# Kernel optimization log

Measured on AMD Instinct MI355X. Metric: run time of the kernel, lower is better.

Reference implementation:

```python
import jax, jax.numpy as jnp
import numpy as np

N = 50000      # n_points (== n_support, non-strided)
H = 32         # neighbors per point
IN_F = 128
OUT_F = 256
MID = OUT_F // 4   # bottleneck width = 64
K = 15         # kernel points
RADIUS = 2.0
KP_EXTENT = 1.2 * RADIUS / 5.0  # config.KP_extent * radius / density_parameter
EPS = 1e-6
SLOPE = 0.1


def _wvar(k, size):
    # weight_variable: normal(scale=sqrt(2/size[-1])), zeroed outside 2*std
    std = np.sqrt(2.0 / size[-1])
    w = jax.random.normal(k, size, jnp.float32) * std
    return jnp.where(jnp.abs(w) > 2.0 * std, 0.0, w)


def setup_inputs():
    key = jax.random.key(0)
    ks = jax.random.split(key, 12)
    query_points = jax.random.uniform(ks[0], (N, 3), jnp.float32)
    support_points = query_points  # non-strided: same cloud
    neighbors_indices = jax.random.randint(ks[1], (N, H), 0, N, jnp.int32)
    features = jax.random.normal(ks[2], (N, IN_F), jnp.float32)
    kp = (jax.random.uniform(ks[3], (K, 3), jnp.float32) * 2.0 - 1.0) * (0.66 * KP_EXTENT)
    kernel_points = kp.at[0].set(0.0)  # fixed_kernel_points='center'
    w1 = _wvar(ks[4], (IN_F, MID))
    kw = _wvar(ks[5], (K, MID, MID))
    w3 = _wvar(ks[6], (MID, OUT_F))
    ws = _wvar(ks[7], (IN_F, OUT_F))
    def bnp(k, c):
        k1, k2 = jax.random.split(k)
        g = jax.random.uniform(k1, (c,), jnp.float32, 0.75, 1.25)
        b = jax.random.normal(k2, (c,), jnp.float32) * 0.1
        return g, b
    g1, b1 = bnp(ks[8], MID)
    g2, b2 = bnp(ks[9], MID)
    g3, b3 = bnp(ks[10], OUT_F)
    gs, bs = bnp(ks[11], OUT_F)
    return dict(query_points=query_points, support_points=support_points,
                neighbors_indices=neighbors_indices, features=features,
                kernel_points=kernel_points, w1=w1, g1=g1, b1=b1,
                kw=kw, g2=g2, b2=b2, w3=w3, g3=g3, b3=b3, ws=ws, gs=gs, bs=bs)


def _bn(x, g, b):
    # BatchNorm1d in training mode: batch statistics over points, biased var
    m = jnp.mean(x, 0)
    v = jnp.var(x, 0)
    return g * (x - m) * jax.lax.rsqrt(v + EPS) + b


def _lrelu(x):
    return jnp.where(x >= 0, x, SLOPE * x)


def _unary(x, w, g, b):
    return _lrelu(_bn(x @ w, g, b))


def _kpconv(q, s, inds, f, kp, kw):
    # pad support with a far shadow point and features with a zero row (faithful to KPConv)
    s_pad = jnp.concatenate([s, jnp.full((1, 3), 1e6, s.dtype)], 0)
    f_pad = jnp.concatenate([f, jnp.zeros((1, f.shape[1]), f.dtype)], 0)
    neigh = s_pad[inds]                        # [n,h,3] gather
    d = neigh - q[:, None, :]                  # [n,h,3]
    sq = jnp.sum((d[:, :, None, :] - kp[None, None, :, :]) ** 2, -1)  # [n,h,K]
    dist = jnp.sqrt(jnp.maximum(sq, 1e-12))
    infl = jnp.maximum(0.0, 1.0 - dist / KP_EXTENT)   # 'linear' KP_influence
    nf = f_pad[inds]                           # [n,h,d] gather
    wf = jnp.einsum('nhk,nhd->nkd', infl, nf)  # aggregate over neighbors
    return jnp.einsum('nkd,kdo->no', wf, kw)   # 'sum' aggregation over kernel pts


def reference(query_points, support_points, neighbors_indices, features, kernel_points,
              w1, g1, b1, kw, g2, b2, w3, g3, b3, ws, gs, bs):
    x = _unary(features, w1, g1, b1)                                     # conv1
    x = _lrelu(_bn(_kpconv(query_points, support_points, neighbors_indices,
                           x, kernel_points, kw), g2, b2))               # conv2 (KPConv)
    x = _unary(x, w3, g3, b3)                                            # conv3
    sc = _unary(features, ws, gs, bs)                                    # shortcut (non-strided)
    return _lrelu(sc + x)
```

## Files before the change

kernel.cpp:

```cpp
#include <hip/hip_runtime.h>

#define NPTS 50000
#define HN 32
#define INF1 128
#define OUTF3 256
#define MIDF 64
#define KP 15
#define EPSV 1e-6f
#define SLOPE 0.1f
#define KPE 0.48f
#define INVN (1.f / 50000.f)

typedef __attribute__((ext_vector_type(8))) short short8;
typedef __attribute__((ext_vector_type(4))) float float4v;
typedef unsigned short ushort;
typedef unsigned long long ull;

__device__ inline ushort f2bf(float f) {
    union { float f; unsigned u; } v; v.f = f;
    unsigned r = v.u + 0x7fff + ((v.u >> 16) & 1);
    return (ushort)(r >> 16);
}
__device__ inline float bf2f(ushort u) {
    union { unsigned u; float f; } v; v.u = ((unsigned)u) << 16;
    return v.f;
}
__device__ inline unsigned cvt_pk_bf16(float lo, float hi) {
    unsigned r;
    asm("v_cvt_pk_bf16_f32 %0, %1, %2" : "=v"(r) : "v"(lo), "v"(hi));
    return r;
}


__global__ __launch_bounds__(256)
void k_repack_all(const float* __restrict__ w1, const float* __restrict__ wsw,
                  ushort* __restrict__ wpC,
                  const float* __restrict__ kw, ushort* __restrict__ wpk,
                  const float* __restrict__ w3, ushort* __restrict__ wp3) {
    int id = blockIdx.x * 256 + threadIdx.x;
    if (id < 5120) {
        int l = id & 63;
        int nt = (id >> 6) % 20, s = id / 1280;
        int n = nt * 16 + (l & 15);
        int k0 = s * 32 + ((l >> 4) & 3) * 8;
#pragma unroll
        for (int j = 0; j < 8; j++) {
            float v = (n < 64) ? w1[(k0 + j) * 64 + n] : wsw[(k0 + j) * 256 + (n - 64)];
            wpC[id * 8 + j] = f2bf(v);
        }
    } else if (id < 13312) {
        int id2 = id - 5120;
        int l2 = id2 & 63;
        int nt = (id2 >> 6) & 3, s = id2 >> 8;
        int n = nt * 16 + (l2 & 15);
        int kd0 = s * 32 + ((l2 >> 4) & 3) * 8;
#pragma unroll
        for (int j = 0; j < 8; j++) {
            int kd = kd0 + j, d = kd >> 4, kk = kd & 15;
            float v = (kk < KP) ? kw[kk * 4096 + d * 64 + n] : 0.f;
            wpk[id2 * 8 + j] = f2bf(v);
        }
    } else if (id < 15360) {
        int id3 = id - 13312;
        int l3 = id3 & 63;
        int nt = (id3 >> 6) % 16, s = id3 / 1024;
        int n = nt * 16 + (l3 & 15);
        int k0 = s * 32 + ((l3 >> 4) & 3) * 8;
#pragma unroll
        for (int j = 0; j < 8; j++)
            wp3[id3 * 8 + j] = f2bf(w3[(k0 + j) * 256 + n]);
    }
}

__global__ __launch_bounds__(256)
void k_conv1sc(const float* __restrict__ feat, const ushort* __restrict__ WpC,
               ushort* __restrict__ x1raw, ushort* __restrict__ scb,
               float* __restrict__ Sa1, float* __restrict__ Sq1,
               float* __restrict__ SaS, float* __restrict__ SqS, int M) {
    __shared__ float sred[320], qred[320];
    int t = threadIdx.x;
    int w = t >> 6, l = t & 63;
    int dl = l & 15, q4 = l >> 4;

    for (int c = t; c < 320; c += 256) { sred[c] = 0.f; qred[c] = 0.f; }
    __syncthreads();

    int m0 = blockIdx.x * 64 + w * 16;
    int row = m0 + dl;
    long arow = (row < M) ? row : (M - 1);
    const float* ap0 = feat + arow * INF1 + q4 * 8;
    short8 afr[4];
#pragma unroll
    for (int s = 0; s < 4; s++) {
        float4 a0 = *(const float4*)(ap0 + s * 32);
        float4 a1 = *(const float4*)(ap0 + s * 32 + 4);
        union { short8 v; unsigned d[4]; } au;
        au.d[0] = cvt_pk_bf16(a0.x, a0.y);
        au.d[1] = cvt_pk_bf16(a0.z, a0.w);
        au.d[2] = cvt_pk_bf16(a1.x, a1.y);
        au.d[3] = cvt_pk_bf16(a1.z, a1.w);
        afr[s] = au.v;
    }
    const short8* Bp = (const short8*)WpC + l;
    int rb = q4 * 4;
#pragma unroll
    for (int half = 0; half < 2; half++) {
        float4v acc[10];
#pragma unroll
        for (int j = 0; j < 10; j++) acc[j] = (float4v){0.f, 0.f, 0.f, 0.f};
#pragma unroll
        for (int s = 0; s < 4; s++)
#pragma unroll
            for (int j = 0; j < 10; j++) {
                short8 bf = Bp[(s * 20 + half * 10 + j) * 64];
                acc[j] = __builtin_amdgcn_mfma_f32_16x16x32_bf16(afr[s], bf, acc[j], 0, 0, 0);
            }
#pragma unroll
        for (int r = 0; r < 4; r++) {
            int rr = m0 + rb + r;
            if (rr < M) {
                if (half == 0) {
                    uint2 pk;
                    pk.x = cvt_pk_bf16(acc[0][r], acc[1][r]);
                    pk.y = cvt_pk_bf16(acc[2][r], acc[3][r]);
                    *(uint2*)(x1raw + (long)rr * 64 + 4 * dl) = pk;
#pragma unroll
                    for (int j = 4; j < 10; j++)
                        scb[(long)rr * 256 + (j * 16 + dl - 64)] = f2bf(acc[j][r]);
                } else {
#pragma unroll
                    for (int j = 0; j < 10; j++)
                        scb[(long)rr * 256 + ((10 + j) * 16 + dl - 64)] = f2bf(acc[j][r]);
                }
            }
        }
#pragma unroll
        for (int j = 0; j < 10; j++) {
            float s = 0.f, q = 0.f;
#pragma unroll
            for (int r = 0; r < 4; r++) {
                float v = ((m0 + rb + r) < M) ? acc[j][r] : 0.f;
                s += v; q += v * v;
            }
            s += __shfl_xor(s, 16); s += __shfl_xor(s, 32);
            q += __shfl_xor(q, 16); q += __shfl_xor(q, 32);
            if (q4 == 0) {
                atomicAdd(&sred[(half * 10 + j) * 16 + dl], s);
                atomicAdd(&qred[(half * 10 + j) * 16 + dl], q);
            }
        }
    }
    __syncthreads();
    for (int c = t; c < 320; c += 256) {
        if (c < 64) { atomicAdd(&Sa1[c], sred[c]); atomicAdd(&Sq1[c], qred[c]); }
        else        { atomicAdd(&SaS[c - 64], sred[c]); atomicAdd(&SqS[c - 64], qred[c]); }
    }
}

__global__ __launch_bounds__(256)
void k_bnx(const ushort* __restrict__ X, ushort* __restrict__ Y,
           const float* __restrict__ Sa, const float* __restrict__ Sq,
           const float* __restrict__ g, const float* __restrict__ b) {
    __shared__ float sc[64], sh[64];
    int t = threadIdx.x;
    if (t < 64) {
        float m = Sa[t] * INVN;
        float v = Sq[t] * INVN - m * m;
        float s = g[t] * rsqrtf(v + EPSV);
        sc[t] = s; sh[t] = b[t] - s * m;
    }
    __syncthreads();
    int i = blockIdx.x * 256 + t;
    long base = (long)i * 4;
    int dlp = i & 15;
    ull vin = *(const ull*)(X + base);
    float vv[4];
#pragma unroll
    for (int j = 0; j < 4; j++) {
        int c = j * 16 + dlp;
        float f = bf2f((ushort)((vin >> (16 * j)) & 0xffff));
        float v = f * sc[c] + sh[c];
        vv[j] = (v >= 0.f) ? v : SLOPE * v;
    }
    uint2 vo;
    vo.x = cvt_pk_bf16(vv[0], vv[1]);
    vo.y = cvt_pk_bf16(vv[2], vv[3]);
    *(uint2*)(Y + base) = vo;
}

__global__ __launch_bounds__(256)
void k_kpconv(const float* __restrict__ qpts, const float* __restrict__ spts,
              const int* __restrict__ nbr, const ushort* __restrict__ x1b,
              const float* __restrict__ kpp, const ushort* __restrict__ kwp,
              ushort* __restrict__ y, float* __restrict__ Sa, float* __restrict__ Sq) {
    __shared__ __align__(16) ushort wfs[16][1032];
    __shared__ float posd[4][4][3][HN];

    int t = threadIdx.x;
    int w = t >> 6, l = t & 63;
    int dl = l & 15, q4 = l >> 4;

    int kmin = (dl < KP) ? dl : (KP - 1);
    float kx = kpp[kmin * 3 + 0], ky = kpp[kmin * 3 + 1], kz = kpp[kmin * 3 + 2];

    int nb = blockIdx.x * 16 + w * 4;

    int idg[4][8];
#pragma unroll
    for (int pp = 0; pp < 4; pp++) {
        const int4* np = (const int4*)(nbr + (long)(nb + pp) * HN + q4 * 8);
        int4 ia = np[0], ib = np[1];
        idg[pp][0] = ia.x; idg[pp][1] = ia.y; idg[pp][2] = ia.z; idg[pp][3] = ia.w;
        idg[pp][4] = ib.x; idg[pp][5] = ib.y; idg[pp][6] = ib.z; idg[pp][7] = ib.w;
    }

    {
        int hh = l & 31, hf = l >> 5;
        float dx[2], dy[2], dz[2];
#pragma unroll
        for (int p2 = 0; p2 < 2; p2++) {
            int pp = hf * 2 + p2;
            int idx = nbr[(long)(nb + pp) * HN + hh];
            dx[p2] = spts[(long)idx * 3 + 0] - qpts[(nb + pp) * 3 + 0];
            dy[p2] = spts[(long)idx * 3 + 1] - qpts[(nb + pp) * 3 + 1];
            dz[p2] = spts[(long)idx * 3 + 2] - qpts[(nb + pp) * 3 + 2];
        }
#pragma unroll
        for (int p2 = 0; p2 < 2; p2++) {
            int pp = hf * 2 + p2;
            posd[w][pp][0][hh] = dx[p2];
            posd[w][pp][1][hh] = dy[p2];
            posd[w][pp][2][hh] = dz[p2];
        }
    }

    uint2 rj[4][8];
#pragma unroll
    for (int pp = 0; pp < 4; pp++)
#pragma unroll
        for (int j = 0; j < 8; j++)
            rj[pp][j] = *(const uint2*)(x1b + (long)idg[pp][j] * MIDF + 4 * dl);

#pragma unroll
    for (int pp = 0; pp < 4; pp++) {
        union { float4 v; float f[4]; } px0, px1, py0, py1, pz0, pz1;
        px0.v = *(const float4*)&posd[w][pp][0][q4 * 8];
        px1.v = *(const float4*)&posd[w][pp][0][q4 * 8 + 4];
        py0.v = *(const float4*)&posd[w][pp][1][q4 * 8];
        py1.v = *(const float4*)&posd[w][pp][1][q4 * 8 + 4];
        pz0.v = *(const float4*)&posd[w][pp][2][q4 * 8];
        pz1.v = *(const float4*)&posd[w][pp][2][q4 * 8 + 4];

        float inf[8];
#pragma unroll
        for (int j = 0; j < 8; j++) {
            float ex = ((j < 4) ? px0.f[j & 3] : px1.f[j & 3]) - kx;
            float ey = ((j < 4) ? py0.f[j & 3] : py1.f[j & 3]) - ky;
            float ez = ((j < 4) ? pz0.f[j & 3] : pz1.f[j & 3]) - kz;
            float sq = ex * ex + ey * ey + ez * ez;
            float dist = sqrtf(fmaxf(sq, 1e-12f));
            inf[j] = fmaxf(0.f, 1.f - dist * (1.f / KPE));
        }
        union { short8 v; unsigned d2[4]; } afr;
#pragma unroll
        for (int jj = 0; jj < 4; jj++)
            afr.d2[jj] = cvt_pk_bf16(inf[2 * jj], inf[2 * jj + 1]);

        union { short8 v; unsigned d[4]; } bfr[4];
#pragma unroll
        for (int dj = 0; dj < 4; dj++) {
            unsigned a_lo = rj[pp][2 * dj].x, b_lo = rj[pp][2 * dj + 1].x;
            unsigned a_hi = rj[pp][2 * dj].y, b_hi = rj[pp][2 * dj + 1].y;
            bfr[0].d[dj] = __builtin_amdgcn_perm(b_lo, a_lo, 0x05040100u);
            bfr[1].d[dj] = __builtin_amdgcn_perm(b_lo, a_lo, 0x07060302u);
            bfr[2].d[dj] = __builtin_amdgcn_perm(b_hi, a_hi, 0x05040100u);
            bfr[3].d[dj] = __builtin_amdgcn_perm(b_hi, a_hi, 0x07060302u);
        }

        float4v wfa[4];
#pragma unroll
        for (int nt = 0; nt < 4; nt++)
            wfa[nt] = __builtin_amdgcn_mfma_f32_16x16x32_bf16(
                afr.v, bfr[nt].v, (float4v){0.f, 0.f, 0.f, 0.f}, 0, 0, 0);

        int p = w * 4 + pp;
#pragma unroll
        for (int nt = 0; nt < 4; nt++) {
            uint2 pk;
            pk.x = cvt_pk_bf16(wfa[nt][0], wfa[nt][1]);
            pk.y = cvt_pk_bf16(wfa[nt][2], wfa[nt][3]);
            *(uint2*)(&wfs[p][(nt * 16 + dl) * 16 + q4 * 4]) = pk;
        }
    }

    const short8* Bq = (const short8*)kwp + l;
    short8 bc0 = Bq[(0 * 4 + w) * 64];
    short8 bc1 = Bq[(1 * 4 + w) * 64];
    __syncthreads();

    float4v acc0 = (float4v){0.f, 0.f, 0.f, 0.f};
    float4v acc1 = (float4v){0.f, 0.f, 0.f, 0.f};
    const ushort* arow = &wfs[dl][0] + q4 * 8;
#pragma unroll
    for (int s = 0; s < 32; s += 2) {
        short8 bn0, bn1;
        if (s < 30) {
            bn0 = Bq[((s + 2) * 4 + w) * 64];
            bn1 = Bq[((s + 3) * 4 + w) * 64];
        }
        short8 a0 = *(const short8*)(arow + s * 32);
        short8 a1 = *(const short8*)(arow + (s + 1) * 32);
        acc0 = __builtin_amdgcn_mfma_f32_16x16x32_bf16(a0, bc0, acc0, 0, 0, 0);
        acc1 = __builtin_amdgcn_mfma_f32_16x16x32_bf16(a1, bc1, acc1, 0, 0, 0);
        bc0 = bn0; bc1 = bn1;
    }
    float4v acc = acc0 + acc1;

    int o = w * 16 + dl;
    float s = 0.f, q = 0.f;
#pragma unroll
    for (int r = 0; r < 4; r++) {
        float v = acc[r];
        y[(long)(blockIdx.x * 16 + q4 * 4 + r) * MIDF + o] = f2bf(v);
        s += v; q += v * v;
    }
    s += __shfl_xor(s, 16); s += __shfl_xor(s, 32);
    q += __shfl_xor(q, 16); q += __shfl_xor(q, 32);
    if (q4 == 0) {
        atomicAdd(&Sa[o], s);
        atomicAdd(&Sq[o], q);
    }
}

__global__ __launch_bounds__(256)
void k_conv3(const ushort* __restrict__ x2raw, const ushort* __restrict__ Wp,
             ushort* __restrict__ x3b,
             const float* __restrict__ Sa2, const float* __restrict__ Sq2,
             const float* __restrict__ g2, const float* __restrict__ b2,
             float* __restrict__ Sa3, float* __restrict__ Sq3, int M) {
    __shared__ float sred[256], qred[256];
    __shared__ float scs[64], shs[64];
    int t = threadIdx.x;
    int w = t >> 6, l = t & 63;
    int dl = l & 15, q4 = l >> 4;

    if (t < 64) {
        float m = Sa2[t] * INVN;
        float v = Sq2[t] * INVN - m * m;
        float s = g2[t] * rsqrtf(v + EPSV);
        scs[t] = s; shs[t] = b2[t] - s * m;
    }
    sred[t] = 0.f; qred[t] = 0.f;
    __syncthreads();

    int m0 = blockIdx.x * 64 + w * 16;
    int row = m0 + dl;
    long arow = (row < M) ? row : (M - 1);
    const ushort* ap0 = x2raw + arow * MIDF + q4 * 8;
    short8 au2[2];
#pragma unroll
    for (int s = 0; s < 2; s++) {
        union { short8 v; ushort u[8]; } raw;
        union { short8 v; unsigned d[4]; } cv;
        raw.v = *(const short8*)(ap0 + s * 32);
        float fv[8];
#pragma unroll
        for (int e = 0; e < 8; e++) {
            int d = s * 32 + q4 * 8 + e;
            float f = bf2f(raw.u[e]) * scs[d] + shs[d];
            fv[e] = (f >= 0.f) ? f : SLOPE * f;
        }
#pragma unroll
        for (int e2 = 0; e2 < 4; e2++)
            cv.d[e2] = cvt_pk_bf16(fv[2 * e2], fv[2 * e2 + 1]);
        au2[s] = cv.v;
    }
    const short8* Bp = (const short8*)Wp + l;
    int rb = q4 * 4;
#pragma unroll
    for (int half = 0; half < 2; half++) {
        float4v acc[8];
#pragma unroll
        for (int j = 0; j < 8; j++) acc[j] = (float4v){0.f, 0.f, 0.f, 0.f};
#pragma unroll
        for (int s = 0; s < 2; s++)
#pragma unroll
            for (int j = 0; j < 8; j++) {
                short8 bf = Bp[(s * 16 + half * 8 + j) * 64];
                acc[j] = __builtin_amdgcn_mfma_f32_16x16x32_bf16(au2[s], bf, acc[j], 0, 0, 0);
            }
#pragma unroll
        for (int r = 0; r < 4; r++) {
            int rr = m0 + rb + r;
            if (rr < M) {
#pragma unroll
                for (int j = 0; j < 8; j++)
                    x3b[(long)rr * 256 + (half * 8 + j) * 16 + dl] = f2bf(acc[j][r]);
            }
        }
#pragma unroll
        for (int j = 0; j < 8; j++) {
            float s = 0.f, q = 0.f;
#pragma unroll
            for (int r = 0; r < 4; r++) {
                float v = ((m0 + rb + r) < M) ? acc[j][r] : 0.f;
                s += v; q += v * v;
            }
            s += __shfl_xor(s, 16); s += __shfl_xor(s, 32);
            q += __shfl_xor(q, 16); q += __shfl_xor(q, 32);
            if (q4 == 0) {
                atomicAdd(&sred[(half * 8 + j) * 16 + dl], s);
                atomicAdd(&qred[(half * 8 + j) * 16 + dl], q);
            }
        }
    }
    __syncthreads();
    atomicAdd(&Sa3[t], sred[t]);
    atomicAdd(&Sq3[t], qred[t]);
}

__global__ __launch_bounds__(256)
void k_final(const ushort* __restrict__ x3b, const ushort* __restrict__ scb,
             float* __restrict__ out,
             const float* __restrict__ a3, const float* __restrict__ q3,
             const float* __restrict__ g3, const float* __restrict__ b3,
             const float* __restrict__ aS, const float* __restrict__ qS,
             const float* __restrict__ gs, const float* __restrict__ bs) {
    __shared__ float s3[256], h3[256], sS[256], hS[256];
    int t = threadIdx.x;
    {
        float m = a3[t] * INVN;
        float v = q3[t] * INVN - m * m;
        float s = g3[t] * rsqrtf(v + EPSV);
        s3[t] = s; h3[t] = b3[t] - s * m;
        m = aS[t] * INVN;
        v = qS[t] * INVN - m * m;
        s = gs[t] * rsqrtf(v + EPSV);
        sS[t] = s; hS[t] = bs[t] - s * m;
    }
    __syncthreads();
    long i = (long)(blockIdx.x * 256 + t) * 4;
    int c0 = (int)(i & 255);
    ull va = *(const ull*)(x3b + i);
    ull vb = *(const ull*)(scb + i);
    float r[4];
#pragma unroll
    for (int j = 0; j < 4; j++) {
        int c = c0 + j;
        float x = bf2f((ushort)((va >> (16 * j)) & 0xffff)) * s3[c] + h3[c];
        x = (x >= 0.f) ? x : SLOPE * x;
        float sc = bf2f((ushort)((vb >> (16 * j)) & 0xffff)) * sS[c] + hS[c];
        sc = (sc >= 0.f) ? sc : SLOPE * sc;
        float v = x + sc;
        r[j] = (v >= 0.f) ? v : SLOPE * v;
    }
    *(float4*)(out + i) = (float4){r[0], r[1], r[2], r[3]};
}

extern "C" void kernel_launch(void* const* d_in, const int* in_sizes, int n_in,
                              void* d_out, int out_size, void* d_ws, size_t ws_size,
                              hipStream_t stream) {
    const float* qp   = (const float*)d_in[0];
    const float* sp   = (const float*)d_in[1];
    const int*   nbr  = (const int*)d_in[2];
    const float* feat = (const float*)d_in[3];
    const float* kpp  = (const float*)d_in[4];
    const float* w1   = (const float*)d_in[5];
    const float* g1   = (const float*)d_in[6];
    const float* b1   = (const float*)d_in[7];
    const float* kw   = (const float*)d_in[8];
    const float* g2   = (const float*)d_in[9];
    const float* b2   = (const float*)d_in[10];
    const float* w3   = (const float*)d_in[11];
    const float* g3   = (const float*)d_in[12];
    const float* b3   = (const float*)d_in[13];
    const float* wsw  = (const float*)d_in[14];
    const float* gs   = (const float*)d_in[15];
    const float* bs   = (const float*)d_in[16];
    float* out = (float*)d_out;

    char* base = (char*)d_ws;
    ushort* x1raw = (ushort*)(base + 0);
    ushort* x1b   = (ushort*)(base + 6400000);
    ushort* x2raw = (ushort*)(base + 12800000);
    ushort* x3b   = (ushort*)(base + 19200000);
    ushort* scb   = (ushort*)(base + 44800000);
    ushort* wpC   = (ushort*)(base + 70400000);
    ushort* wpk   = (ushort*)(base + 70481920);
    ushort* wp3   = (ushort*)(base + 70612992);
    float*  st    = (float*)(base + 70645760);
    float* acc1 = st,       *q1 = st + 64;
    float* acc2 = st + 128, *q2 = st + 192;
    float* acc3 = st + 256, *q3 = st + 512;
    float* accS = st + 768, *qS = st + 1024;

    hipMemsetAsync(st, 0, 1280 * sizeof(float), stream);

    k_repack_all<<<60, 256, 0, stream>>>(w1, wsw, wpC, kw, wpk, w3, wp3);

    k_conv1sc<<<782, 256, 0, stream>>>(feat, wpC, x1raw, scb, acc1, q1, accS, qS, NPTS);
    k_bnx<<<3125, 256, 0, stream>>>(x1raw, x1b, acc1, q1, g1, b1);

    k_kpconv<<<NPTS / 16, 256, 0, stream>>>(qp, sp, nbr, x1b, kpp, wpk, x2raw, acc2, q2);

    k_conv3<<<782, 256, 0, stream>>>(x2raw, wp3, x3b, acc2, q2, g2, b2, acc3, q3, NPTS);

    k_final<<<12500, 256, 0, stream>>>(x3b, scb, out, acc3, q3, g3, b3, accS, qS, gs, bs);
}
```

Baseline: 299.2 us.

## Recompute conv3 GEMM in final kernel instead of storing x3 intermediate

Splits conv3 into a stats-only pass that computes the GEMM and accumulates batch-norm sums without writing x3. A second pass recomputes the same small GEMM, stages the tile in shared memory, and applies BN, leaky ReLU and the residual add with the shortcut directly. This removes the 25.6MB bf16 write and re-read of x3 in exchange for doing the 64x256 GEMM twice. The 32KB shared tile may also reduce occupancy.

Measured after the change: 298.3 us. No clear change (-0.3%).

```diff
diff --git a/kernel.cpp b/kernel.cpp
--- a/kernel.cpp
+++ b/kernel.cpp
@@ -333,11 +333,10 @@
 }
 
 __global__ __launch_bounds__(256)
-void k_conv3(const ushort* __restrict__ x2raw, const ushort* __restrict__ Wp,
-             ushort* __restrict__ x3b,
-             const float* __restrict__ Sa2, const float* __restrict__ Sq2,
-             const float* __restrict__ g2, const float* __restrict__ b2,
-             float* __restrict__ Sa3, float* __restrict__ Sq3, int M) {
+void k_conv3stats(const ushort* __restrict__ x2raw, const ushort* __restrict__ Wp,
+                  const float* __restrict__ Sa2, const float* __restrict__ Sq2,
+                  const float* __restrict__ g2, const float* __restrict__ b2,
+                  float* __restrict__ Sa3, float* __restrict__ Sq3, int M) {
     __shared__ float sred[256], qred[256];
     __shared__ float scs[64], shs[64];
     int t = threadIdx.x;
@@ -390,15 +389,6 @@
                 acc[j] = __builtin_amdgcn_mfma_f32_16x16x32_bf16(au2[s], bf, acc[j], 0, 0, 0);
             }
 #pragma unroll
-        for (int r = 0; r < 4; r++) {
-            int rr = m0 + rb + r;
-            if (rr < M) {
-#pragma unroll
-                for (int j = 0; j < 8; j++)
-                    x3b[(long)rr * 256 + (half * 8 + j) * 16 + dl] = f2bf(acc[j][r]);
-            }
-        }
-#pragma unroll
         for (int j = 0; j < 8; j++) {
             float s = 0.f, q = 0.f;
 #pragma unroll
@@ -420,14 +410,28 @@
 }
 
 __global__ __launch_bounds__(256)
-void k_final(const ushort* __restrict__ x3b, const ushort* __restrict__ scb,
-             float* __restrict__ out,
-             const float* __restrict__ a3, const float* __restrict__ q3,
-             const float* __restrict__ g3, const float* __restrict__ b3,
-             const float* __restrict__ aS, const float* __restrict__ qS,
-             const float* __restrict__ gs, const float* __restrict__ bs) {
+void k_conv3final(const ushort* __restrict__ x2raw, const ushort* __restrict__ Wp,
+                  const ushort* __restrict__ scb, float* __restrict__ out,
+                  const float* __restrict__ Sa2, const float* __restrict__ Sq2,
+                  const float* __restrict__ g2, const float* __restrict__ b2,
+                  const float* __restrict__ a3, const float* __restrict__ q3,
+                  const float* __restrict__ g3, const float* __restrict__ b3,
+                  const float* __restrict__ aS, const float* __restrict__ qS,
+                  const float* __restrict__ gs, const float* __restrict__ bs,
+                  int M) {
+    __shared__ float scs[64], shs[64];
     __shared__ float s3[256], h3[256], sS[256], hS[256];
+    __shared__ __align__(8) ushort x3t[64][256];
     int t = threadIdx.x;
+    int w = t >> 6, l = t & 63;
+    int dl = l & 15, q4 = l >> 4;
+
+    if (t < 64) {
+        float m = Sa2[t] * INVN;
+        float v = Sq2[t] * INVN - m * m;
+        float s = g2[t] * rsqrtf(v + EPSV);
+        scs[t] = s; shs[t] = b2[t] - s * m;
+    }
     {
         float m = a3[t] * INVN;
         float v = q3[t] * INVN - m * m;
@@ -439,22 +443,76 @@
         sS[t] = s; hS[t] = bs[t] - s * m;
     }
     __syncthreads();
-    long i = (long)(blockIdx.x * 256 + t) * 4;
-    int c0 = (int)(i & 255);
-    ull va = *(const ull*)(x3b + i);
-    ull vb = *(const ull*)(scb + i);
-    float r[4];
-#pragma unroll
-    for (int j = 0; j < 4; j++) {
-        int c = c0 + j;
-        float x = bf2f((ushort)((va >> (16 * j)) & 0xffff)) * s3[c] + h3[c];
-        x = (x >= 0.f) ? x : SLOPE * x;
-        float sc = bf2f((ushort)((vb >> (16 * j)) & 0xffff)) * sS[c] + hS[c];
-        sc = (sc >= 0.f) ? sc : SLOPE * sc;
-        float v = x + sc;
-        r[j] = (v >= 0.f) ? v : SLOPE * v;
-    }
-    *(float4*)(out + i) = (float4){r[0], r[1], r[2], r[3]};
+
+    int m0 = blockIdx.x * 64 + w * 16;
+    int row = m0 + dl;
+    long arow = (row < M) ? row : (M - 1);
+    const ushort* ap0 = x2raw + arow * MIDF + q4 * 8;
+    short8 au2[2];
+#pragma unroll
+    for (int s = 0; s < 2; s++) {
+        union { short8 v; ushort u[8]; } raw;
+        union { short8 v; unsigned d[4]; } cv;
+        raw.v = *(const short8*)(ap0 + s * 32);
+        float fv[8];
+#pragma unroll
+        for (int e = 0; e < 8; e++) {
+            int d = s * 32 + q4 * 8 + e;
+            float f = bf2f(raw.u[e]) * scs[d] + shs[d];
+            fv[e] = (f >= 0.f) ? f : SLOPE * f;
+        }
+#pragma unroll
+        for (int e2 = 0; e2 < 4; e2++)
+            cv.d[e2] = cvt_pk_bf16(fv[2 * e2], fv[2 * e2 + 1]);
+        au2[s] = cv.v;
+    }
+    const short8* Bp = (const short8*)Wp + l;
+    int rb = q4 * 4;
+#pragma unroll
+    for (int half = 0; half < 2; half++) {
+        float4v acc[8];
+#pragma unroll
+        for (int j = 0; j < 8; j++) acc[j] = (float4v){0.f, 0.f, 0.f, 0.f};
+#pragma unroll
+        for (int s = 0; s < 2; s++)
+#pragma unroll
+            for (int j = 0; j < 8; j++) {
+                short8 bf = Bp[(s * 16 + half * 8 + j) * 64];
+                acc[j] = __builtin_amdgcn_mfma_f32_16x16x32_bf16(au2[s], bf, acc[j], 0, 0, 0);
+            }
+#pragma unroll
+        for (int r = 0; r < 4; r++) {
+            int lrow = w * 16 + rb + r;
+#pragma unroll
+            for (int j = 0; j < 8; j++)
+                x3t[lrow][(half * 8 + j) * 16 + dl] = f2bf(acc[j][r]);
+        }
+    }
+    __syncthreads();
+
+#pragma unroll
+    for (int it = 0; it < 16; it++) {
+        int e = it * 1024 + t * 4;
+        int lrow = e >> 8;
+        int grow = blockIdx.x * 64 + lrow;
+        if (grow < M) {
+            int col = e & 255;
+            ull va = *(const ull*)&x3t[lrow][col];
+            ull vb = *(const ull*)(scb + (long)grow * 256 + col);
+            float r[4];
+#pragma unroll
+            for (int j = 0; j < 4; j++) {
+                int c = col + j;
+                float x = bf2f((ushort)((va >> (16 * j)) & 0xffff)) * s3[c] + h3[c];
+                x = (x >= 0.f) ? x : SLOPE * x;
+                float sc = bf2f((ushort)((vb >> (16 * j)) & 0xffff)) * sS[c] + hS[c];
+                sc = (sc >= 0.f) ? sc : SLOPE * sc;
+                float v = x + sc;
+                r[j] = (v >= 0.f) ? v : SLOPE * v;
+            }
+            *(float4*)(out + (long)grow * 256 + col) = (float4){r[0], r[1], r[2], r[3]};
+        }
+    }
 }
 
 extern "C" void kernel_launch(void* const* d_in, const int* in_sizes, int n_in,
@@ -483,7 +541,6 @@
     ushort* x1raw = (ushort*)(base + 0);
     ushort* x1b   = (ushort*)(base + 6400000);
     ushort* x2raw = (ushort*)(base + 12800000);
-    ushort* x3b   = (ushort*)(base + 19200000);
     ushort* scb   = (ushort*)(base + 44800000);
     ushort* wpC   = (ushort*)(base + 70400000);
     ushort* wpk   = (ushort*)(base + 70481920);
@@ -503,7 +560,8 @@
 
     k_kpconv<<<NPTS / 16, 256, 0, stream>>>(qp, sp, nbr, x1b, kpp, wpk, x2raw, acc2, q2);
 
-    k_conv3<<<782, 256, 0, stream>>>(x2raw, wp3, x3b, acc2, q2, g2, b2, acc3, q3, NPTS);
-
-    k_final<<<12500, 256, 0, stream>>>(x3b, scb, out, acc3, q3, g3, b3, accS, qS, gs, bs);
-}
+    k_conv3stats<<<782, 256, 0, stream>>>(x2raw, wp3, acc2, q2, g2, b2, acc3, q3, NPTS);
+    k_conv3final<<<782, 256, 0, stream>>>(x2raw, wp3, scb, out,
+                                          acc2, q2, g2, b2, acc3, q3,
+                                          g3, b3, accS, qS, gs, bs, NPTS);
+}
```
